# Optimization experiments

Measured on AMD Instinct MI355X. Metric: run time of the kernel, lower is better.

Reference implementation:

```python
import jax, jax.numpy as jnp
import numpy as np

TOPK = 10
NUM_CLASSES = 80
ALPHA = 0.5
BETA = 6.0
EPS = 1e-16


def _iou_xyxy(b1, b2):
    # b1, b2 broadcastable [..., 4] in xyxy; matches bbox_iou(xywh=False, CIoU=False)
    b1_x1, b1_y1, b1_x2, b1_y2 = b1[..., 0], b1[..., 1], b1[..., 2], b1[..., 3]
    b2_x1, b2_y1, b2_x2, b2_y2 = b2[..., 0], b2[..., 1], b2[..., 2], b2[..., 3]
    inter = jnp.clip(jnp.minimum(b1_x2, b2_x2) - jnp.maximum(b1_x1, b2_x1), 0) * \
            jnp.clip(jnp.minimum(b1_y2, b2_y2) - jnp.maximum(b1_y1, b2_y1), 0)
    w1, h1 = b1_x2 - b1_x1, b1_y2 - b1_y1 + EPS
    w2, h2 = b2_x2 - b2_x1, b2_y2 - b2_y1 + EPS
    union = w1 * h1 + w2 * h2 - inter + EPS
    return inter / union


def _assign_one(pd_s, pd_b, gt_l, gt_b, m, anc):
    # pd_s [A,C], pd_b [A,4], gt_l [N,1], gt_b [N,4], m [N,1] bool, anc [A,2]
    A = pd_s.shape[0]
    N = gt_l.shape[0]
    valid = m[:, 0]                                  # [N] padded-gt mask
    labels = gt_l[:, 0]                              # [N]
    scores = pd_s[:, labels]                         # [A,N] gather per-gt class score
    ious = _iou_xyxy(gt_b[None, :, :], pd_b[:, None, :])   # [A,N]
    align = scores ** ALPHA * ious ** BETA           # [A,N]
    # anchor-center-inside-gt test
    lt = anc[:, None, :] - gt_b[None, :, :2]         # [A,N,2]
    rb = gt_b[None, :, 2:] - anc[:, None, :]         # [A,N,2]
    in_gts = jnp.concatenate([lt, rb], axis=-1).min(axis=-1) > 0  # [A,N]
    amf = align * in_gts                             # align_metric_filter
    amf = jnp.where(valid[None, :], amf, 0.0)        # padded gts contribute nothing
    # top-k anchors per gt (over anchor dim)
    topk_idx = jax.lax.top_k(amf.T, TOPK)[1]         # [N,TOPK]
    mask_topk = jnp.zeros((N, A), dtype=bool).at[jnp.arange(N)[:, None], topk_idx].set(True).T  # [A,N]
    mask_pos = mask_topk & in_gts & valid[None, :]   # [A,N]
    fg = mask_pos.any(axis=1)                        # [A]
    # argmax over valid gts (padded columns pushed below any valid amf >= 0)
    amf_arg = jnp.where(valid[None, :], amf, -1.0)
    gt_idx = jnp.argmax(amf_arg, axis=1)             # [A]
    t_labels = jnp.where(fg, labels[gt_idx], NUM_CLASSES).astype(jnp.int32)
    t_bboxes = jnp.where(fg[:, None], gt_b[gt_idx], 0.0)
    am_max = jnp.clip(jnp.max(amf_arg, axis=1), 0.0)  # [A]
    BIG = jnp.float32(1e30)
    mn = jnp.min(jnp.where(fg, am_max, BIG))
    mx = jnp.max(jnp.where(fg, am_max, -BIG))
    norm = (am_max - mn) / (mx - mn + 1e-9)
    onehot = jax.nn.one_hot(t_labels, NUM_CLASSES, dtype=pd_s.dtype)  # label==C -> all-zero row
    t_scores = jnp.where(fg[:, None], onehot * norm[:, None], 0.0)
    return t_labels, t_bboxes, t_scores, fg


def setup_inputs() -> dict:
    key = jax.random.key(0)
    B, A, N, C = 32, 8400, 64, NUM_CLASSES
    ks = jax.random.split(key, 8)
    pd_scores = jax.random.uniform(ks[0], (B, A, C), dtype=jnp.float32)
    xy1 = jax.random.uniform(ks[1], (B, A, 2), dtype=jnp.float32) * 600.0
    wh = jax.random.uniform(ks[2], (B, A, 2), dtype=jnp.float32) * 60.0 + 4.0
    pd_bboxes = jnp.concatenate([xy1, xy1 + wh], axis=-1)
    anc_points = jax.random.uniform(ks[3], (A, 2), dtype=jnp.float32) * 640.0
    gxy1 = jax.random.uniform(ks[4], (B, N, 2), dtype=jnp.float32) * 500.0
    gwh = jax.random.uniform(ks[5], (B, N, 2), dtype=jnp.float32) * 140.0 + 20.0
    gt_bboxes = jnp.concatenate([gxy1, gxy1 + gwh], axis=-1)
    gt_labels = jax.random.randint(ks[6], (B, N, 1), 0, C, dtype=jnp.int32)
    counts = jax.random.randint(ks[7], (B,), 1, N + 1)
    mask_gt = (jnp.arange(N)[None, :] < counts[:, None])[..., None]  # [B,N,1] bool
    return {"pd_scores": pd_scores, "pd_bboxes": pd_bboxes, "anc_points": anc_points,
            "gt_labels": gt_labels, "gt_bboxes": gt_bboxes, "mask_gt": mask_gt}


def reference(pd_scores, pd_bboxes, anc_points, gt_labels, gt_bboxes, mask_gt):
    return jax.vmap(_assign_one, in_axes=(0, 0, 0, 0, 0, None))(
        pd_scores, pd_bboxes, gt_labels, gt_bboxes, mask_gt, anc_points)
```

## Files before the change

kernel.cpp:

```cpp
#include <hip/hip_runtime.h>

#define A_N 8400
#define B_N 32
#define NGT 64
#define NC  80
#define BA  (B_N * A_N)
#define NCOL (B_N * NGT)

typedef float f4 __attribute__((ext_vector_type(4)));

__global__ __launch_bounds__(256) void k_init(int* __restrict__ cnts,
                                              unsigned* __restrict__ mn_g,
                                              unsigned* __restrict__ mx_g) {
  int tid = threadIdx.x;
  for (int i = tid; i < NCOL; i += 256) cnts[i] = 0;
  if (tid < B_N) {
    mn_g[tid] = __float_as_uint(1e30f);
    mx_g[tid] = 0u;
  }
}

__global__ __launch_bounds__(256) void k_pairs(
    const float* __restrict__ pd_s, const float* __restrict__ pd_b,
    const float* __restrict__ anc, const int* __restrict__ gt_l,
    const float* __restrict__ gt_b, const int* __restrict__ mgt,
    unsigned long long* __restrict__ lists, int* __restrict__ cnts, int cap,
    unsigned long long* __restrict__ recs) {
#pragma clang fp contract(off)
  int b = blockIdx.y, tid = threadIdx.x;
  int a0 = blockIdx.x * 256, a = a0 + tid;
  bool av = a < A_N;

  __shared__ float4 gb_s[NGT];
  __shared__ int lab_s[NGT];
  __shared__ float4 pb_s[256];
  __shared__ unsigned long long key_s[256];
  __shared__ unsigned short wl[256 * 32];
  __shared__ int wl_cnt;
  __shared__ int cnt_sh;

  if (tid < NGT) {
    gb_s[tid] = ((const float4*)gt_b)[b * NGT + tid];
    lab_s[tid] = gt_l[b * NGT + tid];
    unsigned long long m = __ballot(mgt[b * NGT + tid] != 0);
    if (tid == 0) cnt_sh = __popcll(m);
  }
  float4 pb = av ? ((const float4*)pd_b)[(size_t)b * A_N + a]
                 : make_float4(0.f, 0.f, 0.f, 0.f);
  float2 ap = av ? ((const float2*)anc)[a] : make_float2(-1e30f, -1e30f);
  pb_s[tid] = pb;
  key_s[tid] = (unsigned long long)(63 << 1);
  if (tid == 0) wl_cnt = 0;
  __syncthreads();
  int cnt = cnt_sh;

  for (int g0 = 0; g0 < cnt; g0 += 32) {
    int ge = (g0 + 32 < cnt) ? g0 + 32 : cnt;
    if (av) {
      for (int n = g0; n < ge; n++) {
        float4 gb = gb_s[n];
        float mn = fminf(fminf(ap.x - gb.x, ap.y - gb.y),
                         fminf(gb.z - ap.x, gb.w - ap.y));
        float iwr = fminf(gb.z, pb.z) - fmaxf(gb.x, pb.x);
        float ihr = fminf(gb.w, pb.w) - fmaxf(gb.y, pb.y);
        if (mn > 0.0f && iwr > 0.0f && ihr > 0.0f) {
          int p = atomicAdd(&wl_cnt, 1);
          wl[p] = (unsigned short)((tid << 6) | (n & 63));
        }
      }
    }
    __syncthreads();
    int m = wl_cnt;
    for (int i = tid; i < m; i += 256) {
      int e = wl[i];
      int al = e >> 6, n = e & 63;
      int ag = a0 + al;
      float4 gb = gb_s[n];
      float4 pbl = pb_s[al];
      float iw = fmaxf(fminf(gb.z, pbl.z) - fmaxf(gb.x, pbl.x), 0.0f);
      float ih = fmaxf(fminf(gb.w, pbl.w) - fmaxf(gb.y, pbl.y), 0.0f);
      float inter = iw * ih;
      float w1 = gb.z - gb.x, h1 = (gb.w - gb.y) + 1e-16f;
      float w2 = pbl.z - pbl.x, h2 = (pbl.w - pbl.y) + 1e-16f;
      float uni = ((w1 * h1 + w2 * h2) - inter) + 1e-16f;
      float iou = inter / uni;
      float sc = pd_s[((size_t)b * A_N + ag) * NC + (size_t)lab_s[n]];
      float v = sqrtf(sc) * powf(iou, 6.0f);
      if (v > 0.0f) {
        unsigned vb = __float_as_uint(v);
        int col = b * NGT + n;
        int pos = atomicAdd(&cnts[col], 1);
        if (pos < cap) {
          lists[(size_t)col * cap + pos] =
              ((unsigned long long)vb << 32) |
              (unsigned long long)(0xFFFFFFFFu - (unsigned)ag);
        }
        atomicMax(&key_s[al], ((unsigned long long)vb << 32) |
                                  (unsigned long long)((63 - n) << 1));
      }
    }
    __syncthreads();
    if (tid == 0) wl_cnt = 0;
    __syncthreads();
  }

  if (av) recs[(size_t)b * A_N + a] = key_s[tid];
}

__global__ __launch_bounds__(64) void k_topk(
    const unsigned long long* __restrict__ lists, const int* __restrict__ cnts,
    int cap, const int* __restrict__ mgt, const float* __restrict__ anc,
    const float* __restrict__ gt_b, unsigned long long* __restrict__ recs,
    unsigned* __restrict__ mn_g, unsigned* __restrict__ mx_g) {
  int b = blockIdx.x, n = blockIdx.y, tid = threadIdx.x;
  if (mgt[b * NGT + n] == 0) return;
  int col = b * NGT + n;
  int P = cnts[col];
  if (P > cap) P = cap;
  const unsigned long long* list = lists + (size_t)col * cap;
  unsigned* recw = (unsigned*)recs;

  const unsigned MN_ID = __float_as_uint(1e30f);
  unsigned loc_mn = MN_ID, loc_mx = 0u;

  if (P >= 10) {
    unsigned long long top[10];
#pragma unroll
    for (int j = 0; j < 10; j++) top[j] = 0ull;
    for (int i = tid; i < P; i += 64) {
      unsigned long long key = list[i];
#pragma unroll
      for (int j = 0; j < 10; j++) {
        if (key > top[j]) { unsigned long long t = top[j]; top[j] = key; key = t; }
      }
    }
    for (int r = 0; r < 10; r++) {
      unsigned long long g = top[0];
#pragma unroll
      for (int off = 32; off >= 1; off >>= 1) {
        unsigned long long o = __shfl_xor(g, off, 64);
        g = (o > g) ? o : g;
      }
      if (top[0] == g) {
#pragma unroll
        for (int j = 0; j < 9; j++) top[j] = top[j + 1];
        top[9] = 0ull;
      }
      if (tid == r) {
        size_t idx = (size_t)b * A_N +
                     (size_t)(0xFFFFFFFFu - (unsigned)(g & 0xFFFFFFFFull));
        atomicOr(&recw[2 * idx], 1u);
        unsigned u = recw[2 * idx + 1];
        loc_mn = (u < loc_mn) ? u : loc_mn;
        loc_mx = (u > loc_mx) ? u : loc_mx;
      }
    }
  } else {
    int my_a = -1;
    if (tid < P)
      my_a = (int)(0xFFFFFFFFu - (unsigned)(list[tid] & 0xFFFFFFFFull));
    if (tid < P) {
      size_t idx = (size_t)b * A_N + my_a;
      atomicOr(&recw[2 * idx], 1u);
      unsigned u = recw[2 * idx + 1];
      loc_mn = (u < loc_mn) ? u : loc_mn;
      loc_mx = (u > loc_mx) ? u : loc_mx;
    }
    bool is_pos = false;
    for (int i = 0; i < P; i++) {
      int ai = __shfl(my_a, i, 64);
      is_pos |= (ai == tid);
    }
    bool cand = (tid < 19) && !is_pos;
    unsigned long long fm = __ballot(cand);
    int rank = __popcll(fm & ((1ull << tid) - 1ull));
    if (cand && rank < 10 - P) {
      float4 gb = ((const float4*)gt_b)[b * NGT + n];
      float2 ap = ((const float2*)anc)[tid];
      float mn = fminf(fminf(ap.x - gb.x, ap.y - gb.y),
                       fminf(gb.z - ap.x, gb.w - ap.y));
      if (mn > 0.0f) {
        size_t idx = (size_t)b * A_N + tid;
        atomicOr(&recw[2 * idx], 1u);
        unsigned u = recw[2 * idx + 1];
        loc_mn = (u < loc_mn) ? u : loc_mn;
        loc_mx = (u > loc_mx) ? u : loc_mx;
      }
    }
  }

#pragma unroll
  for (int off = 32; off >= 1; off >>= 1) {
    unsigned o1 = __shfl_xor(loc_mn, off, 64);
    loc_mn = (o1 < loc_mn) ? o1 : loc_mn;
    unsigned o2 = __shfl_xor(loc_mx, off, 64);
    loc_mx = (o2 > loc_mx) ? o2 : loc_mx;
  }
  if (tid == 0 && loc_mn != MN_ID) {
    atomicMin(&mn_g[b], loc_mn);
    atomicMax(&mx_g[b], loc_mx);
  }
}

__global__ __launch_bounds__(256) void k_out(
    const int* __restrict__ gt_l, const float* __restrict__ gt_b,
    const unsigned long long* __restrict__ recs,
    const unsigned* __restrict__ mn_g, const unsigned* __restrict__ mx_g,
    float* __restrict__ out) {
  int b = blockIdx.y;
  int tid = threadIdx.x;
  int a0 = blockIdx.x * 256;
  int a = a0 + tid;

  __shared__ int cls_s[256];
  __shared__ float norm_s[256];

  if (a < A_N) {
    size_t i = (size_t)b * A_N + a;
    unsigned long long rec = recs[i];
    bool fg = (rec & 1ull) != 0;
    int bi = 63 - (int)((rec >> 1) & 63ull);
    float amx = __uint_as_float((unsigned)(rec >> 32));
    float mn = __uint_as_float(mn_g[b]);
    float mx = __uint_as_float(mx_g[b]);
    float norm = (amx - mn) / ((mx - mn) + 1e-9f);
    int lab = gt_l[b * NGT + bi];

    __builtin_nontemporal_store(fg ? (float)lab : (float)NC, &out[i]);
    f4 bb;
    if (fg) {
      float4 t = ((const float4*)gt_b)[b * NGT + bi];
      bb.x = t.x; bb.y = t.y; bb.z = t.z; bb.w = t.w;
    } else {
      bb = (f4){0.f, 0.f, 0.f, 0.f};
    }
    __builtin_nontemporal_store(bb, &((f4*)(out + BA))[i]);
    __builtin_nontemporal_store(fg ? 1.0f : 0.0f, &out[(size_t)85 * BA + i]);
    cls_s[tid] = fg ? lab : -1;
    norm_s[tid] = fg ? norm : 0.0f;
  } else {
    cls_s[tid] = -1;
    norm_s[tid] = 0.0f;
  }
  __syncthreads();

  int nA = A_N - a0;
  if (nA > 256) nA = 256;
  f4* dst = (f4*)(out + (size_t)5 * BA + ((size_t)b * A_N + a0) * NC);
  int nvec = nA * (NC / 4);
  for (int t = tid; t < nvec; t += 256) {
    int al = t / (NC / 4);
    int c0 = (t - al * (NC / 4)) * 4;
    int cls = cls_s[al];
    float nv = norm_s[al];
    f4 r;
    r.x = (c0 == cls) ? nv : 0.0f;
    r.y = (c0 + 1 == cls) ? nv : 0.0f;
    r.z = (c0 + 2 == cls) ? nv : 0.0f;
    r.w = (c0 + 3 == cls) ? nv : 0.0f;
    __builtin_nontemporal_store(r, &dst[t]);
  }
}

extern "C" void kernel_launch(void* const* d_in, const int* in_sizes, int n_in,
                              void* d_out, int out_size, void* d_ws,
                              size_t ws_size, hipStream_t stream) {
  const float* pd_s = (const float*)d_in[0];
  const float* pd_b = (const float*)d_in[1];
  const float* anc  = (const float*)d_in[2];
  const int*   gt_l = (const int*)d_in[3];
  const float* gt_b = (const float*)d_in[4];
  const int*   mgt  = (const int*)d_in[5];

  float* out = (float*)d_out;
  char* ws = (char*)d_ws;

  const size_t REC_BYTES = (size_t)BA * 8;
  size_t small_bytes = REC_BYTES + (size_t)NCOL * 4 + 256;
  size_t avail = (ws_size > small_bytes) ? (ws_size - small_bytes) : 0;
  int cap = (int)(avail / ((size_t)NCOL * 8));
  if (cap > 4096) cap = 4096;
  if (cap < 1) cap = 1;

  unsigned long long* lists = (unsigned long long*)ws;
  char* sb = ws + (size_t)NCOL * 8 * cap;
  unsigned long long* recs = (unsigned long long*)sb;
  int*      cnts = (int*)(sb + REC_BYTES);
  unsigned* mn_g = (unsigned*)(sb + REC_BYTES + (size_t)NCOL * 4);
  unsigned* mx_g = mn_g + B_N;

  dim3 g2((A_N + 255) / 256, B_N);
  k_init<<<1, 256, 0, stream>>>(cnts, mn_g, mx_g);
  k_pairs<<<g2, 256, 0, stream>>>(pd_s, pd_b, anc, gt_l, gt_b, mgt, lists,
                                  cnts, cap, recs);
  k_topk<<<dim3(B_N, NGT), 64, 0, stream>>>(lists, cnts, cap, mgt, anc, gt_b,
                                            recs, mn_g, mx_g);
  k_out<<<g2, 256, 0, stream>>>(gt_l, gt_b, recs, mn_g, mx_g, out);
}
```

Measured before the change: 185.4 us.

## Zero output with memset and scatter foreground values; single-pass pair worklist

The output kernel no longer writes every element of the dense one-hot score tensor and the bbox and fg arrays itself. A hipMemsetAsync now clears that region, and the finishing kernel writes only the foreground entries: the bbox, the fg flag and one scattered normalized score. Separately, the pair kernel builds its worklist in one pass over all ground truths, with a larger shared-memory buffer, instead of in chunks of 32 with extra barriers. The memset still writes the full region, so the saving depends on whether the memset runs faster than plain kernel stores. The larger shared-memory buffer may also reduce occupancy of the pair kernel.

```diff
diff --git a/kernel.cpp b/kernel.cpp
--- a/kernel.cpp
+++ b/kernel.cpp
@@ -35,7 +35,7 @@
   __shared__ int lab_s[NGT];
   __shared__ float4 pb_s[256];
   __shared__ unsigned long long key_s[256];
-  __shared__ unsigned short wl[256 * 32];
+  __shared__ unsigned short wl[256 * 64];
   __shared__ int wl_cnt;
   __shared__ int cnt_sh;
 
@@ -54,55 +54,51 @@
   __syncthreads();
   int cnt = cnt_sh;
 
-  for (int g0 = 0; g0 < cnt; g0 += 32) {
-    int ge = (g0 + 32 < cnt) ? g0 + 32 : cnt;
-    if (av) {
-      for (int n = g0; n < ge; n++) {
-        float4 gb = gb_s[n];
-        float mn = fminf(fminf(ap.x - gb.x, ap.y - gb.y),
-                         fminf(gb.z - ap.x, gb.w - ap.y));
-        float iwr = fminf(gb.z, pb.z) - fmaxf(gb.x, pb.x);
-        float ihr = fminf(gb.w, pb.w) - fmaxf(gb.y, pb.y);
-        if (mn > 0.0f && iwr > 0.0f && ihr > 0.0f) {
-          int p = atomicAdd(&wl_cnt, 1);
-          wl[p] = (unsigned short)((tid << 6) | (n & 63));
-        }
-      }
-    }
-    __syncthreads();
-    int m = wl_cnt;
-    for (int i = tid; i < m; i += 256) {
-      int e = wl[i];
-      int al = e >> 6, n = e & 63;
-      int ag = a0 + al;
+  if (av) {
+    for (int n = 0; n < cnt; n++) {
       float4 gb = gb_s[n];
-      float4 pbl = pb_s[al];
-      float iw = fmaxf(fminf(gb.z, pbl.z) - fmaxf(gb.x, pbl.x), 0.0f);
-      float ih = fmaxf(fminf(gb.w, pbl.w) - fmaxf(gb.y, pbl.y), 0.0f);
-      float inter = iw * ih;
-      float w1 = gb.z - gb.x, h1 = (gb.w - gb.y) + 1e-16f;
-      float w2 = pbl.z - pbl.x, h2 = (pbl.w - pbl.y) + 1e-16f;
-      float uni = ((w1 * h1 + w2 * h2) - inter) + 1e-16f;
-      float iou = inter / uni;
-      float sc = pd_s[((size_t)b * A_N + ag) * NC + (size_t)lab_s[n]];
-      float v = sqrtf(sc) * powf(iou, 6.0f);
-      if (v > 0.0f) {
-        unsigned vb = __float_as_uint(v);
-        int col = b * NGT + n;
-        int pos = atomicAdd(&cnts[col], 1);
-        if (pos < cap) {
-          lists[(size_t)col * cap + pos] =
-              ((unsigned long long)vb << 32) |
-              (unsigned long long)(0xFFFFFFFFu - (unsigned)ag);
-        }
-        atomicMax(&key_s[al], ((unsigned long long)vb << 32) |
-                                  (unsigned long long)((63 - n) << 1));
-      }
-    }
-    __syncthreads();
-    if (tid == 0) wl_cnt = 0;
-    __syncthreads();
-  }
+      float mn = fminf(fminf(ap.x - gb.x, ap.y - gb.y),
+                       fminf(gb.z - ap.x, gb.w - ap.y));
+      float iwr = fminf(gb.z, pb.z) - fmaxf(gb.x, pb.x);
+      float ihr = fminf(gb.w, pb.w) - fmaxf(gb.y, pb.y);
+      if (mn > 0.0f && iwr > 0.0f && ihr > 0.0f) {
+        int p = atomicAdd(&wl_cnt, 1);
+        wl[p] = (unsigned short)((tid << 6) | n);
+      }
+    }
+  }
+  __syncthreads();
+  int m = wl_cnt;
+
+  for (int i = tid; i < m; i += 256) {
+    int e = wl[i];
+    int al = e >> 6, n = e & 63;
+    int ag = a0 + al;
+    float4 gb = gb_s[n];
+    float4 pbl = pb_s[al];
+    float iw = fmaxf(fminf(gb.z, pbl.z) - fmaxf(gb.x, pbl.x), 0.0f);
+    float ih = fmaxf(fminf(gb.w, pbl.w) - fmaxf(gb.y, pbl.y), 0.0f);
+    float inter = iw * ih;
+    float w1 = gb.z - gb.x, h1 = (gb.w - gb.y) + 1e-16f;
+    float w2 = pbl.z - pbl.x, h2 = (pbl.w - pbl.y) + 1e-16f;
+    float uni = ((w1 * h1 + w2 * h2) - inter) + 1e-16f;
+    float iou = inter / uni;
+    float sc = pd_s[((size_t)b * A_N + ag) * NC + (size_t)lab_s[n]];
+    float v = sqrtf(sc) * powf(iou, 6.0f);
+    if (v > 0.0f) {
+      unsigned vb = __float_as_uint(v);
+      int col = b * NGT + n;
+      int pos = atomicAdd(&cnts[col], 1);
+      if (pos < cap) {
+        lists[(size_t)col * cap + pos] =
+            ((unsigned long long)vb << 32) |
+            (unsigned long long)(0xFFFFFFFFu - (unsigned)ag);
+      }
+      atomicMax(&key_s[al], ((unsigned long long)vb << 32) |
+                                (unsigned long long)((63 - n) << 1));
+    }
+  }
+  __syncthreads();
 
   if (av) recs[(size_t)b * A_N + a] = key_s[tid];
 }
@@ -202,63 +198,31 @@
   }
 }
 
-__global__ __launch_bounds__(256) void k_out(
+__global__ __launch_bounds__(256) void k_fin(
     const int* __restrict__ gt_l, const float* __restrict__ gt_b,
     const unsigned long long* __restrict__ recs,
     const unsigned* __restrict__ mn_g, const unsigned* __restrict__ mx_g,
     float* __restrict__ out) {
   int b = blockIdx.y;
-  int tid = threadIdx.x;
-  int a0 = blockIdx.x * 256;
-  int a = a0 + tid;
-
-  __shared__ int cls_s[256];
-  __shared__ float norm_s[256];
-
-  if (a < A_N) {
-    size_t i = (size_t)b * A_N + a;
-    unsigned long long rec = recs[i];
-    bool fg = (rec & 1ull) != 0;
-    int bi = 63 - (int)((rec >> 1) & 63ull);
+  int a = blockIdx.x * 256 + threadIdx.x;
+  if (a >= A_N) return;
+  size_t i = (size_t)b * A_N + a;
+  unsigned long long rec = recs[i];
+  bool fg = (rec & 1ull) != 0;
+  int bi = 63 - (int)((rec >> 1) & 63ull);
+  int lab = gt_l[b * NGT + bi];
+
+  out[i] = fg ? (float)lab : (float)NC;
+  if (fg) {
     float amx = __uint_as_float((unsigned)(rec >> 32));
     float mn = __uint_as_float(mn_g[b]);
     float mx = __uint_as_float(mx_g[b]);
     float norm = (amx - mn) / ((mx - mn) + 1e-9f);
-    int lab = gt_l[b * NGT + bi];
-
-    __builtin_nontemporal_store(fg ? (float)lab : (float)NC, &out[i]);
-    f4 bb;
-    if (fg) {
-      float4 t = ((const float4*)gt_b)[b * NGT + bi];
-      bb.x = t.x; bb.y = t.y; bb.z = t.z; bb.w = t.w;
-    } else {
-      bb = (f4){0.f, 0.f, 0.f, 0.f};
-    }
-    __builtin_nontemporal_store(bb, &((f4*)(out + BA))[i]);
-    __builtin_nontemporal_store(fg ? 1.0f : 0.0f, &out[(size_t)85 * BA + i]);
-    cls_s[tid] = fg ? lab : -1;
-    norm_s[tid] = fg ? norm : 0.0f;
-  } else {
-    cls_s[tid] = -1;
-    norm_s[tid] = 0.0f;
-  }
-  __syncthreads();
-
-  int nA = A_N - a0;
-  if (nA > 256) nA = 256;
-  f4* dst = (f4*)(out + (size_t)5 * BA + ((size_t)b * A_N + a0) * NC);
-  int nvec = nA * (NC / 4);
-  for (int t = tid; t < nvec; t += 256) {
-    int al = t / (NC / 4);
-    int c0 = (t - al * (NC / 4)) * 4;
-    int cls = cls_s[al];
-    float nv = norm_s[al];
-    f4 r;
-    r.x = (c0 == cls) ? nv : 0.0f;
-    r.y = (c0 + 1 == cls) ? nv : 0.0f;
-    r.z = (c0 + 2 == cls) ? nv : 0.0f;
-    r.w = (c0 + 3 == cls) ? nv : 0.0f;
-    __builtin_nontemporal_store(r, &dst[t]);
+    float4 t = ((const float4*)gt_b)[b * NGT + bi];
+    f4 bb = {t.x, t.y, t.z, t.w};
+    ((f4*)(out + BA))[i] = bb;
+    out[(size_t)85 * BA + i] = 1.0f;
+    out[(size_t)5 * BA + i * NC + (size_t)lab] = norm;
   }
 }
 
@@ -289,11 +253,13 @@
   unsigned* mn_g = (unsigned*)(sb + REC_BYTES + (size_t)NCOL * 4);
   unsigned* mx_g = mn_g + B_N;
 
+  hipMemsetAsync(out + BA, 0, (size_t)85 * BA * 4, stream);
+
   dim3 g2((A_N + 255) / 256, B_N);
   k_init<<<1, 256, 0, stream>>>(cnts, mn_g, mx_g);
   k_pairs<<<g2, 256, 0, stream>>>(pd_s, pd_b, anc, gt_l, gt_b, mgt, lists,
                                   cnts, cap, recs);
   k_topk<<<dim3(B_N, NGT), 64, 0, stream>>>(lists, cnts, cap, mgt, anc, gt_b,
                                             recs, mn_g, mx_g);
-  k_out<<<g2, 256, 0, stream>>>(gt_l, gt_b, recs, mn_g, mx_g, out);
-}
+  k_fin<<<g2, 256, 0, stream>>>(gt_l, gt_b, recs, mn_g, mx_g, out);
+}
```

New measurement: 182.9 us. Within noise of the previous version (-1.3%).
